# Kernel tuning notes

Measured on AMD Instinct MI355X. Metric: run time of the kernel, lower is better.

The kernel has to match this reference:

```python
import jax, jax.numpy as jnp
import numpy as np

N = 100000   # nodes
E = 1600000  # edges
IN = 128     # input_dim
H = 64       # hidden_dim
OUT = 2      # output_dim
G = 64       # number of graphs in the batch


def setup_inputs() -> dict:
    key = jax.random.key(0)
    ks = jax.random.split(key, 12)
    x = jax.random.normal(ks[0], (N, IN), dtype=jnp.float32)
    edge_index = jax.random.randint(ks[1], (2, E), 0, N, dtype=jnp.int64)
    batch = jnp.sort(jax.random.randint(ks[2], (N,), 0, G, dtype=jnp.int64))
    s = 0.05
    return {
        "x": x,
        "edge_index": edge_index,
        "batch": batch,
        "W1": jax.random.normal(ks[3], (IN, H), dtype=jnp.float32) * s,
        "b1": jnp.zeros((H,), dtype=jnp.float32),
        "W2": jax.random.normal(ks[4], (H, H), dtype=jnp.float32) * s,
        "b2": jnp.zeros((H,), dtype=jnp.float32),
        "W3": jax.random.normal(ks[5], (H, H), dtype=jnp.float32) * s,
        "b3": jnp.zeros((H,), dtype=jnp.float32),
        "Wm1": jax.random.normal(ks[6], (H, H), dtype=jnp.float32) * s,
        "bm1": jnp.zeros((H,), dtype=jnp.float32),
        "Wm2": jax.random.normal(ks[7], (H, OUT), dtype=jnpp.float32) * s if False else jax.random.normal(ks[7], (H, OUT), dtype=jnp.float32) * s,
        "bm2": jnp.zeros((OUT,), dtype=jnp.float32),
    }


def _gcn_conv(x, W, b, src, dst, norm, n_nodes):
    # PyG GCNConv: h = x @ W; message = norm * h[src]; scatter-add at dst; + bias
    h = x @ W                                  # [N, H]
    msg = h[src] * norm[:, None]               # [E+N, H] gather + scale
    out = jax.ops.segment_sum(msg, dst, num_segments=n_nodes)
    return out + b


def reference(x, edge_index, batch, W1, b1, W2, b2, W3, b3, Wm1, bm1, Wm2, bm2):
    n = x.shape[0]
    # add self-loops (PyG GCNConv default add_self_loops=True)
    loop = jnp.arange(n, dtype=edge_index.dtype)
    src = jnp.concatenate([edge_index[0], loop])
    dst = jnp.concatenate([edge_index[1], loop])
    # symmetric normalization deg^-1/2 (deg over target nodes, incl. self-loops)
    deg = jax.ops.segment_sum(jnp.ones_like(dst, dtype=x.dtype), dst, num_segments=n)
    dinv = jnp.where(deg > 0, jax.lax.rsqrt(deg), 0.0)
    norm = dinv[src] * dinv[dst]               # [E+N]

    h = jax.nn.relu(_gcn_conv(x, W1, b1, src, dst, norm, n))   # dropout: eval -> identity
    h = jax.nn.relu(_gcn_conv(h, W2, b2, src, dst, norm, n))
    h = jax.nn.relu(_gcn_conv(h, W3, b3, src, dst, norm, n))

    # global_mean_pool over batch ids
    sums = jax.ops.segment_sum(h, batch, num_segments=G)       # [G, H]
    cnts = jax.ops.segment_sum(jnp.ones((n,), dtype=h.dtype), batch, num_segments=G)
    pooled = sums / jnp.maximum(cnts, 1.0)[:, None]

    # MLP head: Linear -> ReLU -> (Dropout eval) -> Linear
    z = jax.nn.relu(pooled @ Wm1 + bm1)
    return z @ Wm2 + bm2                                       # [G, OUT]
```

## Files before the change

### kernel.cpp

```cpp
#include <hip/hip_runtime.h>
#include <hip/hip_bf16.h>

#define NNODES 100000
#define NEDGES 1600000
#define IND 128
#define HD 64
#define OUTD 2
#define NG 64
#define BINSHIFT 9
#define BINSZ 512
#define BSTRIDE 12288
#define PB 256

typedef __attribute__((ext_vector_type(8))) short short8v;
typedef __attribute__((ext_vector_type(4))) float floatx4;

static __device__ __forceinline__ unsigned short f2bf(float f) {
    __hip_bfloat16 h = __float2bfloat16(f);
    return *(unsigned short*)&h;
}
static __device__ __forceinline__ float bf2f(unsigned short u) {
    __hip_bfloat16 h = *(__hip_bfloat16*)&u;
    return __bfloat162float(h);
}

__global__ __launch_bounds__(256) void binP_kernel(const int* __restrict__ src,
                                                   const int* __restrict__ dst,
                                                   int* __restrict__ binCount,
                                                   unsigned int* __restrict__ binned,
                                                   int E, int nbins) {
    __shared__ int lh[256];
    __shared__ int lbase[256];
    int t = threadIdx.x;
    lh[t] = 0;
    __syncthreads();
    int ebpb = (E + PB - 1) / PB;
    int e0 = blockIdx.x * ebpb;
    int e1 = min(e0 + ebpb, E);
    for (int e = e0 + t; e < e1; e += 256)
        atomicAdd(&lh[dst[e] >> BINSHIFT], 1);
    __syncthreads();
    int c = lh[t];
    if (t < nbins && c > 0) lbase[t] = atomicAdd(&binCount[t], c);
    lh[t] = 0;
    __syncthreads();
    for (int e = e0 + t; e < e1; e += 256) {
        int d = dst[e];
        int b = d >> BINSHIFT;
        int idx = atomicAdd(&lh[b], 1);
        binned[(size_t)b * BSTRIDE + lbase[b] + idx] =
            ((unsigned int)(d & (BINSZ - 1)) << 17) | (unsigned int)src[e];
    }
}

__global__ __launch_bounds__(256) void binHD_kernel(const unsigned int* __restrict__ binned,
                                                    const int* __restrict__ binCount,
                                                    float* __restrict__ dinv,
                                                    unsigned int* __restrict__ rowinfo,
                                                    int* __restrict__ ssrc, int n) {
    __shared__ int dh[BINSZ];
    __shared__ int rp[BINSZ];
    __shared__ int wsum[4];
    int b = blockIdx.x, t = threadIdx.x;
    int lane = t & 63, wv = t >> 6;
    dh[t] = 0; dh[t + 256] = 0;
    __syncthreads();
    int s0 = b * BSTRIDE;
    int cnt = binCount[b];
    for (int i = t; i < cnt; i += 256)
        atomicAdd(&dh[binned[s0 + i] >> 17], 1);
    __syncthreads();
#pragma unroll
    for (int r = 0; r < 2; r++) {
        int i = t + r * 256;
        int node = (b << BINSHIFT) + i;
        if (node < n) dinv[node] = 1.0f / sqrtf((float)(dh[i] + 1));
    }
    int d0 = dh[2 * t], d1 = dh[2 * t + 1];
    int p = d0 + d1;
    int sc = p;
#pragma unroll
    for (int d = 1; d < 64; d <<= 1) { int v = __shfl_up(sc, d, 64); if (lane >= d) sc += v; }
    if (lane == 63) wsum[wv] = sc;
    __syncthreads();
    int add = 0;
    for (int w2 = 0; w2 < wv; w2++) add += wsum[w2];
    int ex = sc - p + add;
    rp[2 * t]     = ex;
    rp[2 * t + 1] = ex + d0;
    __syncthreads();
#pragma unroll
    for (int r = 0; r < 2; r++) {
        int i = t + r * 256;
        int node = (b << BINSHIFT) + i;
        if (node < n)
            rowinfo[node] = ((unsigned int)(s0 + rp[i]) << 10) |
                            (unsigned int)min(dh[i], 1023);
    }
    __syncthreads();
    for (int i = t; i < cnt; i += 256) {
        unsigned int rec = binned[s0 + i];
        int doff = rec >> 17;
        int s = rec & 0x1FFFF;
        int idx = atomicSub(&dh[doff], 1) - 1;
        ssrc[s0 + rp[doff] + idx] = s;
    }
}

__global__ __launch_bounds__(256) void prep_kernel(const float* __restrict__ W1,
                                                   const float* __restrict__ W2,
                                                   const float* __restrict__ W3,
                                                   unsigned short* __restrict__ WT1,
                                                   unsigned short* __restrict__ WT2,
                                                   unsigned short* __restrict__ WT3,
                                                   const int* __restrict__ batch,
                                                   float* __restrict__ gcnt, int n) {
    int blk = blockIdx.x;
    if (blk < 64) {
        int i = blk * 256 + threadIdx.x;
        if (i < 64 * IND) {
            int nn2 = i / IND, k = i - nn2 * IND;
            WT1[i] = f2bf(W1[k * 64 + nn2]);
        } else if (i < 64 * IND + 64 * HD) {
            int j = i - 64 * IND;
            int nn2 = j / HD, k = j - nn2 * HD;
            WT2[j] = f2bf(W2[k * 64 + nn2]);
        } else {
            int j = i - 64 * IND - 64 * HD;
            int nn2 = j / HD, k = j - nn2 * HD;
            WT3[j] = f2bf(W3[k * 64 + nn2]);
        }
    } else {
        __shared__ float lg[NG];
        int t = threadIdx.x;
        if (t < NG) lg[t] = 0.f;
        __syncthreads();
        int nb2 = gridDim.x - 64;
        int per = (n + nb2 - 1) / nb2;
        int i0 = (blk - 64) * per;
        int i1 = min(i0 + per, n);
        for (int i = i0 + t; i < i1; i += 256)
            atomicAdd(&lg[batch[i]], 1.f);
        __syncthreads();
        if (t < NG) atomicAdd(&gcnt[t], lg[t]);
    }
}

template <int K, bool BF16IN>
__global__ __launch_bounds__(256) void mm_mfma_kernel(const void* __restrict__ Xv,
                                                      const unsigned short* __restrict__ WT,
                                                      const float* __restrict__ dinv,
                                                      unsigned short* __restrict__ Tb, int nn) {
    const int lane = threadIdx.x & 63;
    const int wv   = threadIdx.x >> 6;
    const int nb   = blockIdx.x * 64 + wv * 16;
    if (nb >= nn) return;
    const int col  = lane & 15;
    const int quad = lane >> 4;
    const int m    = min(nb + col, nn - 1);

    floatx4 acc0 = {0.f, 0.f, 0.f, 0.f};
    floatx4 acc1 = {0.f, 0.f, 0.f, 0.f};
    floatx4 acc2 = {0.f, 0.f, 0.f, 0.f};
    floatx4 acc3 = {0.f, 0.f, 0.f, 0.f};

#pragma unroll
    for (int ks = 0; ks < K; ks += 32) {
        const int k0 = ks + quad * 8;
        short8v a;
        if (BF16IN) {
            a = *(const short8v*)((const unsigned short*)Xv + (size_t)m * K + k0);
        } else {
            const float* xr = (const float*)Xv + (size_t)m * K + k0;
            float4 f0 = *(const float4*)(xr);
            float4 f1 = *(const float4*)(xr + 4);
            a[0] = (short)f2bf(f0.x); a[1] = (short)f2bf(f0.y);
            a[2] = (short)f2bf(f0.z); a[3] = (short)f2bf(f0.w);
            a[4] = (short)f2bf(f1.x); a[5] = (short)f2bf(f1.y);
            a[6] = (short)f2bf(f1.z); a[7] = (short)f2bf(f1.w);
        }
        short8v b0 = *(const short8v*)(WT + (size_t)(0  + col) * K + k0);
        short8v b1 = *(const short8v*)(WT + (size_t)(16 + col) * K + k0);
        short8v b2 = *(const short8v*)(WT + (size_t)(32 + col) * K + k0);
        short8v b3 = *(const short8v*)(WT + (size_t)(48 + col) * K + k0);
        acc0 = __builtin_amdgcn_mfma_f32_16x16x32_bf16(a, b0, acc0, 0, 0, 0);
        acc1 = __builtin_amdgcn_mfma_f32_16x16x32_bf16(a, b1, acc1, 0, 0, 0);
        acc2 = __builtin_amdgcn_mfma_f32_16x16x32_bf16(a, b2, acc2, 0, 0, 0);
        acc3 = __builtin_amdgcn_mfma_f32_16x16x32_bf16(a, b3, acc3, 0, 0, 0);
    }

#pragma unroll
    for (int r = 0; r < 4; r++) {
        int node = nb + quad * 4 + r;
        if (node < nn) {
            float sc = dinv[node];
            unsigned short* o = Tb + (size_t)node * 64 + col;
            o[0]  = f2bf(sc * acc0[r]);
            o[16] = f2bf(sc * acc1[r]);
            o[32] = f2bf(sc * acc2[r]);
            o[48] = f2bf(sc * acc3[r]);
        }
    }
}

__global__ __launch_bounds__(256) void agg_kernel(const unsigned short* __restrict__ Tb,
                                                  const unsigned int* __restrict__ rowinfo,
                                                  const int* __restrict__ ssrc,
                                                  const float* __restrict__ dinv,
                                                  const float* __restrict__ bias,
                                                  unsigned short* __restrict__ Ob, int nn) {
    int wave = __builtin_amdgcn_readfirstlane((blockIdx.x * 256 + threadIdx.x) >> 6);
    int lane = threadIdx.x & 63;
    if (wave >= nn) return;
    int n = wave;
    float acc = bf2f(Tb[(size_t)n * 64 + lane]);
    unsigned int info = rowinfo[n];
    int rb = (int)(info >> 10);
    int re = rb + (int)(info & 1023);
    int i = rb;
    for (; i + 16 <= re; i += 16) {
        int s[16];
#pragma unroll
        for (int k = 0; k < 16; k++) s[k] = ssrc[i + k];
        float v[16];
#pragma unroll
        for (int k = 0; k < 16; k++) v[k] = bf2f(Tb[(size_t)s[k] * 64 + lane]);
#pragma unroll
        for (int k = 0; k < 16; k++) acc += v[k];
    }
    for (; i + 4 <= re; i += 4) {
        int s0 = ssrc[i], s1 = ssrc[i + 1], s2 = ssrc[i + 2], s3 = ssrc[i + 3];
        float v0 = bf2f(Tb[(size_t)s0 * 64 + lane]);
        float v1 = bf2f(Tb[(size_t)s1 * 64 + lane]);
        float v2 = bf2f(Tb[(size_t)s2 * 64 + lane]);
        float v3 = bf2f(Tb[(size_t)s3 * 64 + lane]);
        acc += v0; acc += v1; acc += v2; acc += v3;
    }
    for (; i < re; i++)
        acc += bf2f(Tb[(size_t)ssrc[i] * 64 + lane]);
    float o = dinv[n] * acc + bias[lane];
    o = o > 0.f ? o : 0.f;
    Ob[(size_t)n * 64 + lane] = f2bf(o);
}

__global__ __launch_bounds__(256) void pool_kernel(const unsigned short* __restrict__ Hb,
                                                   const int* __restrict__ batch,
                                                   float* __restrict__ pooled, int nn) {
    int wid = (blockIdx.x * 256 + threadIdx.x) >> 6;
    int lane = threadIdx.x & 63;
    int nwaves = (gridDim.x * 256) >> 6;
    int per = (nn + nwaves - 1) / nwaves;
    int n0 = wid * per;
    int n1 = n0 + per; if (n1 > nn) n1 = nn;
    if (n0 >= n1) return;
    int cur = batch[n0];
    float acc = 0.f;
    for (int n = n0; n < n1; ++n) {
        int g = batch[n];
        if (g != cur) {
            atomicAdd(&pooled[cur * 64 + lane], acc);
            acc = 0.f; cur = g;
        }
        acc += bf2f(Hb[(size_t)n * 64 + lane]);
    }
    atomicAdd(&pooled[cur * 64 + lane], acc);
}

__global__ __launch_bounds__(256) void head_kernel(const float* __restrict__ pooled,
                                                   const float* __restrict__ gcnt,
                                                   const float* __restrict__ Wm1,
                                                   const float* __restrict__ bm1,
                                                   const float* __restrict__ Wm2,
                                                   const float* __restrict__ bm2,
                                                   float* __restrict__ out) {
    __shared__ float P[NG * 64];
    __shared__ float Z[NG * 64];
    int tid = threadIdx.x;
    for (int i = tid; i < NG * 64; i += 256) {
        int g = i >> 6;
        float c = gcnt[g];
        c = c > 1.f ? c : 1.f;
        P[i] = pooled[i] / c;
    }
    __syncthreads();
    for (int i = tid; i < NG * 64; i += 256) {
        int g = i >> 6, j = i & 63;
        float a = bm1[j];
#pragma unroll 8
        for (int k = 0; k < 64; ++k) a += P[g * 64 + k] * Wm1[k * 64 + j];
        Z[i] = a > 0.f ? a : 0.f;
    }
    __syncthreads();
    for (int i = tid; i < NG * OUTD; i += 256) {
        int g = i / OUTD, o = i % OUTD;
        float a = bm2[o];
#pragma unroll 8
        for (int k = 0; k < 64; ++k) a += Z[g * 64 + k] * Wm2[k * OUTD + o];
        out[i] = a;
    }
}

extern "C" void kernel_launch(void* const* d_in, const int* in_sizes, int n_in,
                              void* d_out, int out_size, void* d_ws, size_t ws_size,
                              hipStream_t stream) {
    const float* x    = (const float*)d_in[0];
    const int*  edge  = (const int*)d_in[1];
    const int*  batch = (const int*)d_in[2];
    const float* W1 = (const float*)d_in[3];
    const float* b1 = (const float*)d_in[4];
    const float* W2 = (const float*)d_in[5];
    const float* b2 = (const float*)d_in[6];
    const float* W3 = (const float*)d_in[7];
    const float* b3 = (const float*)d_in[8];
    const float* Wm1 = (const float*)d_in[9];
    const float* bm1 = (const float*)d_in[10];
    const float* Wm2 = (const float*)d_in[11];
    const float* bm2 = (const float*)d_in[12];

    const int N_ = in_sizes[2];
    const int E_ = in_sizes[1] / 2;
    const int* src = edge;
    const int* dst = edge + E_;
    const int nbins = (N_ + BINSZ - 1) >> BINSHIFT;

    char* w = (char*)d_ws;
    auto alloc = [&](size_t bytes) -> void* {
        void* p = (void*)w;
        w += (bytes + 255) & ~(size_t)255;
        return p;
    };
    float* dinv   = (float*)alloc((size_t)N_ * 4);
    unsigned int* rowinfo = (unsigned int*)alloc((size_t)N_ * 4);
    float* pooled = (float*)alloc((size_t)(NG * 64 + NG) * 4);
    int*   binCount = (int*)alloc(256 * 4);
    float* gcnt   = pooled + NG * 64;
    int*   ssrc   = (int*)alloc((size_t)nbins * BSTRIDE * 4);
    unsigned int* binned = (unsigned int*)alloc((size_t)nbins * BSTRIDE * 4);
    unsigned short* Tb  = (unsigned short*)alloc((size_t)N_ * 64 * 2);
    unsigned short* hBb = (unsigned short*)alloc((size_t)N_ * 64 * 2);
    unsigned short* WT1 = (unsigned short*)alloc((size_t)64 * IND * 2);
    unsigned short* WT2 = (unsigned short*)alloc((size_t)64 * HD * 2);
    unsigned short* WT3 = (unsigned short*)alloc((size_t)64 * HD * 2);

    hipMemsetAsync(pooled, 0, (size_t)(NG * 64 + NG) * 4 + 256 * 4 + 256, stream);

    binP_kernel<<<PB, 256, 0, stream>>>(src, dst, binCount, binned, E_, nbins);
    binHD_kernel<<<nbins, 256, 0, stream>>>(binned, binCount, dinv, rowinfo, ssrc, N_);

    prep_kernel<<<64 + 16, 256, 0, stream>>>(W1, W2, W3, WT1, WT2, WT3, batch, gcnt, N_);

    const int mmblk = (N_ + 63) / 64;
    const int aggblk = (N_ + 3) / 4;

    mm_mfma_kernel<IND, false><<<mmblk, 256, 0, stream>>>(x, WT1, dinv, Tb, N_);
    agg_kernel<<<aggblk, 256, 0, stream>>>(Tb, rowinfo, ssrc, dinv, b1, hBb, N_);
    mm_mfma_kernel<HD, true><<<mmblk, 256, 0, stream>>>(hBb, WT2, dinv, Tb, N_);
    agg_kernel<<<aggblk, 256, 0, stream>>>(Tb, rowinfo, ssrc, dinv, b2, hBb, N_);
    mm_mfma_kernel<HD, true><<<mmblk, 256, 0, stream>>>(hBb, WT3, dinv, Tb, N_);
    agg_kernel<<<aggblk, 256, 0, stream>>>(Tb, rowinfo, ssrc, dinv, b3, hBb, N_);

    pool_kernel<<<256, 256, 0, stream>>>(hBb, batch, pooled, N_);
    head_kernel<<<1, 256, 0, stream>>>(pooled, gcnt, Wm1, bm1, Wm2, bm2, (float*)d_out);
}
```

Measured before the change: 403.3 us.

## Fuse next-layer 64x64 weight multiply into aggregation epilogue

```diff
diff --git a/kernel.cpp b/kernel.cpp
--- a/kernel.cpp
+++ b/kernel.cpp
@@ -37,15 +37,21 @@
     int ebpb = (E + PB - 1) / PB;
     int e0 = blockIdx.x * ebpb;
     int e1 = min(e0 + ebpb, E);
-    for (int e = e0 + t; e < e1; e += 256)
-        atomicAdd(&lh[dst[e] >> BINSHIFT], 1);
+    int dcache[25];
+    int ec = 0;
+    for (int e = e0 + t; e < e1; e += 256) {
+        int d = dst[e];
+        dcache[ec++] = d;
+        atomicAdd(&lh[d >> BINSHIFT], 1);
+    }
     __syncthreads();
     int c = lh[t];
     if (t < nbins && c > 0) lbase[t] = atomicAdd(&binCount[t], c);
     lh[t] = 0;
     __syncthreads();
+    ec = 0;
     for (int e = e0 + t; e < e1; e += 256) {
-        int d = dst[e];
+        int d = dcache[ec++];
         int b = d >> BINSHIFT;
         int idx = atomicAdd(&lh[b], 1);
         binned[(size_t)b * BSTRIDE + lbase[b] + idx] =
@@ -108,36 +114,22 @@
 }
 
 __global__ __launch_bounds__(256) void prep_kernel(const float* __restrict__ W1,
-                                                   const float* __restrict__ W2,
-                                                   const float* __restrict__ W3,
                                                    unsigned short* __restrict__ WT1,
-                                                   unsigned short* __restrict__ WT2,
-                                                   unsigned short* __restrict__ WT3,
                                                    const int* __restrict__ batch,
                                                    float* __restrict__ gcnt, int n) {
     int blk = blockIdx.x;
-    if (blk < 64) {
+    if (blk < 32) {
         int i = blk * 256 + threadIdx.x;
-        if (i < 64 * IND) {
-            int nn2 = i / IND, k = i - nn2 * IND;
-            WT1[i] = f2bf(W1[k * 64 + nn2]);
-        } else if (i < 64 * IND + 64 * HD) {
-            int j = i - 64 * IND;
-            int nn2 = j / HD, k = j - nn2 * HD;
-            WT2[j] = f2bf(W2[k * 64 + nn2]);
-        } else {
-            int j = i - 64 * IND - 64 * HD;
-            int nn2 = j / HD, k = j - nn2 * HD;
-            WT3[j] = f2bf(W3[k * 64 + nn2]);
-        }
+        int nn2 = i / IND, k = i - nn2 * IND;
+        WT1[i] = f2bf(W1[k * 64 + nn2]);
     } else {
         __shared__ float lg[NG];
         int t = threadIdx.x;
         if (t < NG) lg[t] = 0.f;
         __syncthreads();
-        int nb2 = gridDim.x - 64;
+        int nb2 = gridDim.x - 32;
         int per = (n + nb2 - 1) / nb2;
-        int i0 = (blk - 64) * per;
+        int i0 = (blk - 32) * per;
         int i1 = min(i0 + per, n);
         for (int i = i0 + t; i < i1; i += 256)
             atomicAdd(&lg[batch[i]], 1.f);
@@ -203,12 +195,20 @@
     }
 }
 
+template <bool FUSE>
 __global__ __launch_bounds__(256) void agg_kernel(const unsigned short* __restrict__ Tb,
                                                   const unsigned int* __restrict__ rowinfo,
                                                   const int* __restrict__ ssrc,
                                                   const float* __restrict__ dinv,
                                                   const float* __restrict__ bias,
-                                                  unsigned short* __restrict__ Ob, int nn) {
+                                                  const float* __restrict__ Wn,
+                                                  unsigned short* __restrict__ Out, int nn) {
+    __shared__ float Wl[64 * 64];
+    if (FUSE) {
+        for (int i = threadIdx.x; i < 64 * 16; i += 256)
+            ((float4*)Wl)[i] = ((const float4*)Wn)[i];
+        __syncthreads();
+    }
     int wave = __builtin_amdgcn_readfirstlane((blockIdx.x * 256 + threadIdx.x) >> 6);
     int lane = threadIdx.x & 63;
     if (wave >= nn) return;
@@ -238,9 +238,20 @@
     }
     for (; i < re; i++)
         acc += bf2f(Tb[(size_t)ssrc[i] * 64 + lane]);
-    float o = dinv[n] * acc + bias[lane];
+    float dn = dinv[n];
+    float o = dn * acc + bias[lane];
     o = o > 0.f ? o : 0.f;
-    Ob[(size_t)n * 64 + lane] = f2bf(o);
+    if (FUSE) {
+        float tacc = 0.f;
+#pragma unroll 16
+        for (int k = 0; k < 64; k++) {
+            float ok = __shfl(o, k, 64);
+            tacc += ok * Wl[k * 64 + lane];
+        }
+        Out[(size_t)n * 64 + lane] = f2bf(dn * tacc);
+    } else {
+        Out[(size_t)n * 64 + lane] = f2bf(o);
+    }
 }
 
 __global__ __launch_bounds__(256) void pool_kernel(const unsigned short* __restrict__ Hb,
@@ -337,27 +348,24 @@
     int*   ssrc   = (int*)alloc((size_t)nbins * BSTRIDE * 4);
     unsigned int* binned = (unsigned int*)alloc((size_t)nbins * BSTRIDE * 4);
     unsigned short* Tb  = (unsigned short*)alloc((size_t)N_ * 64 * 2);
+    unsigned short* Tb2 = (unsigned short*)alloc((size_t)N_ * 64 * 2);
     unsigned short* hBb = (unsigned short*)alloc((size_t)N_ * 64 * 2);
     unsigned short* WT1 = (unsigned short*)alloc((size_t)64 * IND * 2);
-    unsigned short* WT2 = (unsigned short*)alloc((size_t)64 * HD * 2);
-    unsigned short* WT3 = (unsigned short*)alloc((size_t)64 * HD * 2);
 
     hipMemsetAsync(pooled, 0, (size_t)(NG * 64 + NG) * 4 + 256 * 4 + 256, stream);
 
     binP_kernel<<<PB, 256, 0, stream>>>(src, dst, binCount, binned, E_, nbins);
     binHD_kernel<<<nbins, 256, 0, stream>>>(binned, binCount, dinv, rowinfo, ssrc, N_);
 
-    prep_kernel<<<64 + 16, 256, 0, stream>>>(W1, W2, W3, WT1, WT2, WT3, batch, gcnt, N_);
+    prep_kernel<<<32 + 16, 256, 0, stream>>>(W1, WT1, batch, gcnt, N_);
 
     const int mmblk = (N_ + 63) / 64;
     const int aggblk = (N_ + 3) / 4;
 
     mm_mfma_kernel<IND, false><<<mmblk, 256, 0, stream>>>(x, WT1, dinv, Tb, N_);
-    agg_kernel<<<aggblk, 256, 0, stream>>>(Tb, rowinfo, ssrc, dinv, b1, hBb, N_);
-    mm_mfma_kernel<HD, true><<<mmblk, 256, 0, stream>>>(hBb, WT2, dinv, Tb, N_);
-    agg_kernel<<<aggblk, 256, 0, stream>>>(Tb, rowinfo, ssrc, dinv, b2, hBb, N_);
-    mm_mfma_kernel<HD, true><<<mmblk, 256, 0, stream>>>(hBb, WT3, dinv, Tb, N_);
-    agg_kernel<<<aggblk, 256, 0, stream>>>(Tb, rowinfo, ssrc, dinv, b3, hBb, N_);
+    agg_kernel<true><<<aggblk, 256, 0, stream>>>(Tb, rowinfo, ssrc, dinv, b1, W2, Tb2, N_);
+    agg_kernel<true><<<aggblk, 256, 0, stream>>>(Tb2, rowinfo, ssrc, dinv, b2, W3, Tb, N_);
+    agg_kernel<false><<<aggblk, 256, 0, stream>>>(Tb, rowinfo, ssrc, dinv, b3, nullptr, hBb, N_);
 
     pool_kernel<<<256, 256, 0, stream>>>(hBb, batch, pooled, N_);
     head_kernel<<<1, 256, 0, stream>>>(pooled, gcnt, Wm1, bm1, Wm2, bm2, (float*)d_out);
```

New measurement: 505.8 us. 1.25x slower.
